# Performance work log

Measured on AMD Instinct MI355X. Metric: run time of the kernel, lower is better.

## Reference

```python
import jax, jax.numpy as jnp
import numpy as np

N_NODES = 50000
N_PAIRS = 400000
F_IN = 5
GCN_DIMS = [32, 64, 128]
MLP_DIMS = [128, 64]


def _lin_init(key, out_d, in_d):
    return jax.random.normal(key, (out_d, in_d), dtype=jnp.float32) / np.sqrt(in_d)


def setup_inputs() -> dict:
    rng = np.random.default_rng(0)
    hi = rng.integers(1, N_NODES, size=N_PAIRS)
    lo = rng.integers(0, 2**31 - 1, size=N_PAIRS) % hi  # lo < hi strictly
    # each undirected pair appears twice per direction (two parallel edges / classes)
    src = np.concatenate([hi, hi, lo, lo]).astype(np.int32)
    dst = np.concatenate([lo, lo, hi, hi]).astype(np.int32)
    edges = jnp.asarray(np.stack([src, dst]))  # [2, 4P]
    detector_labels = jnp.asarray(rng.random(N_NODES) < 0.9)
    key = jax.random.key(0)
    ks = jax.random.split(key, 16)
    x = jax.random.normal(ks[0], (N_NODES, F_IN), dtype=jnp.float32)
    edge_attr = jax.random.uniform(ks[1], (4 * N_PAIRS, 2), dtype=jnp.float32)
    inp = {"x": x, "edges": edges, "edge_attr": edge_attr, "detector_labels": detector_labels}
    dims = [F_IN] + GCN_DIMS
    for i, (di, do) in enumerate(zip(dims[:-1], dims[1:])):
        inp[f"gc{i}_Wrel"] = _lin_init(ks[2 + 3 * i], do, di)
        inp[f"gc{i}_brel"] = jnp.zeros((do,), dtype=jnp.float32)
        inp[f"gc{i}_Wroot"] = _lin_init(ks[3 + 3 * i], do, di)
    mdims = [2 * GCN_DIMS[-1] + 1] + MLP_DIMS
    for i, (di, do) in enumerate(zip(mdims[:-1], mdims[1:])):
        inp[f"fc{i}_W"] = _lin_init(ks[11 + 2 * i], do, di)
        inp[f"fc{i}_b"] = jnp.zeros((do,), dtype=jnp.float32)
    inp["out_W"] = _lin_init(ks[15], 1, MLP_DIMS[-1])
    inp["out_b"] = jnp.zeros((1,), dtype=jnp.float32)
    return inp


def _edge_perm(edges_np, det_np):
    # SplitSyndromes: keep edges with both endpoints in detector set, src > dst,
    # then sort_edge_index (stable lexicographic sort by (src, dst)).
    src, dst = edges_np[0], edges_np[1]
    valid = det_np[src] & det_np[dst] & (src > dst)
    idx = np.where(valid)[0]
    order = np.lexsort((dst[idx], src[idx]))
    return idx[order]


def reference(x, edges, edge_attr, detector_labels,
              gc0_Wrel, gc0_brel, gc0_Wroot,
              gc1_Wrel, gc1_brel, gc1_Wroot,
              gc2_Wrel, gc2_brel, gc2_Wroot,
              fc0_W, fc0_b, fc1_W, fc1_b, out_W, out_b):
    src, dst = edges[0], edges[1]
    w = edge_attr[:, 0] * edge_attr[:, 1]  # GraphConv edge weight
    # GraphConv: lin_rel(sum_j w_ji * x_j) + lin_root(x), ReLU
    for Wrel, brel, Wroot in ((gc0_Wrel, gc0_brel, gc0_Wroot),
                              (gc1_Wrel, gc1_brel, gc1_Wroot),
                              (gc2_Wrel, gc2_brel, gc2_Wroot)):
        agg = jax.ops.segment_sum(x[src] * w[:, None], dst, num_segments=N_NODES)
        x = jax.nn.relu(agg @ Wrel.T + brel + x @ Wroot.T)
    perm = _edge_perm(np.asarray(edges), np.asarray(detector_labels))
    e_src = edges[0, perm]
    e_dst = edges[1, perm]
    ea = edge_attr[perm]  # [M, 2]
    feat = jnp.concatenate([x[e_src], ea[:, :1], x[e_dst]], axis=-1)  # [M, 257]
    for W, b in ((fc0_W, fc0_b), (fc1_W, fc1_b)):
        feat = jax.nn.relu(feat @ W.T + b)
    score = feat @ out_W.T + out_b  # [M, 1]
    pair = jnp.concatenate([score[::2], score[1::2]], axis=1)  # [M/2, 2]
    cls = jnp.stack([ea[::2, 1], ea[1::2, 1]], axis=1)  # [M/2, 2]
    mi = jnp.argmin(pair, axis=1)
    sel = jnp.take_along_axis(pair, mi[:, None], axis=1)[:, 0]
    cls_sel = jnp.take_along_axis(cls, mi[:, None], axis=1)[:, 0]
    edges_out = jnp.stack([e_src[::2], e_dst[::2]])
    return edges_out, jax.nn.sigmoid(sel), cls_sel
```

## Files before the change

kernel.cpp:

```cpp
#include <hip/hip_runtime.h>
#include <hip/hip_bf16.h>
#include <stdint.h>

typedef unsigned long long ull;
typedef unsigned short us;
typedef unsigned char u8;
typedef __attribute__((ext_vector_type(8))) short short8;
typedef __attribute__((ext_vector_type(4))) float f32x4;
#define IDX_BITS 22
#define IDX_MASK 0x3FFFFFu

__device__ __forceinline__ float bfq(float x) {
    return __bfloat162float(__float2bfloat16(x));
}
__device__ __forceinline__ us bfu(float x) {
    __hip_bfloat16 b = __float2bfloat16(x);
    return *(us*)&b;
}
__device__ __forceinline__ float b2f(us u) {
    return __bfloat162float(*(__hip_bfloat16*)&u);
}
__device__ __forceinline__ u8 f2q(float x) {
    x = fminf(fmaxf(x, -448.f), 448.f);
    unsigned int u = __float_as_uint(x);
    unsigned int s = (u >> 24) & 0x80;
    float ax = fabsf(x);
    if (ax < 0.0009765625f) return (u8)s;
    unsigned int au = u & 0x7FFFFFFF;
    int e = (int)(au >> 23) - 127;
    unsigned int m = au & 0x7FFFFF;
    int E = e + 7;
    if (E <= 0) {
        int q = (int)rintf(ax * 512.f);
        if (q >= 8) return (u8)(s | 0x08);
        return (u8)(s | q);
    }
    unsigned int keep = m >> 20;
    unsigned int rest = m & 0xFFFFF;
    keep += (rest > 0x80000u || (rest == 0x80000u && (keep & 1)));
    if (keep == 8) { keep = 0; ++E; }
    if (E >= 16) return (u8)(s | 0x7E);
    return (u8)(s | (E << 3) | keep);
}
__device__ __forceinline__ float q2f(u8 v) {
    int E = (v >> 3) & 0xF, m = v & 7;
    float mag = (E == 0) ? (float)m * 0.001953125f
                         : __uint_as_float((unsigned)(((E + 120) << 23) | (m << 20)));
    return (v & 0x80) ? -mag : mag;
}
__device__ __forceinline__ float ldx(const float* p, size_t i) { return p[i]; }
__device__ __forceinline__ float ldx(const us* p, size_t i) { return b2f(p[i]); }


__global__ void k_det8(const int* __restrict__ src, const int* __restrict__ dst,
                       const u8* __restrict__ det, int P, int gP, int* __restrict__ stats,
                       int* __restrict__ dcnt, int* __restrict__ scnt,
                       int2* __restrict__ rnk, int* __restrict__ vrnk,
                       const float* __restrict__ W1rel, const float* __restrict__ W1root,
                       const float* __restrict__ W2rel, const float* __restrict__ W2root,
                       const float* __restrict__ W3rel, const float* __restrict__ W3root,
                       const float* __restrict__ W0, const float* __restrict__ Wfc1,
                       us* __restrict__ pb1, us* __restrict__ pb2, us* __restrict__ pb3,
                       us* __restrict__ pbP, us* __restrict__ pbQ, us* __restrict__ w1f) {
    if ((int)blockIdx.x >= gP) {
        int gid = (blockIdx.x - gP) * 256 + threadIdx.x;
        const float* Wrel;
        const float* Wroot;
        us* out;
        int idx, FIN, CT;
        if (gid < 1024) { idx = gid; Wrel = W1rel; Wroot = W1root; out = pb1; FIN = 5; CT = 2; }
        else if (gid < 5120) { idx = gid - 1024; Wrel = W2rel; Wroot = W2root; out = pb2; FIN = 32; CT = 4; }
        else if (gid < 21504) { idx = gid - 5120; Wrel = W3rel; Wroot = W3root; out = pb3; FIN = 64; CT = 8; }
        else if (gid < 54272) {
            int i2 = gid - 21504;
            bool isQ = i2 >= 16384;
            int i = i2 & 16383;
            int j = i & 7, l = (i >> 3) & 63, ct = (i >> 9) & 7, ks = i >> 12;
            int k = ks * 32 + ((l >> 4) << 3) + j;
            int col = ct * 16 + (l & 15);
            float v = isQ ? W0[col * 257 + 129 + k] : W0[col * 257 + k];
            (isQ ? pbQ : pbP)[i] = bfu(v);
            return;
        } else if (gid < 62464) {
            int i = gid - 54272;
            int j = i & 7, l = (i >> 3) & 63, ct = (i >> 9) & 3, ks = i >> 11;
            int k = ks * 32 + ((l >> 4) << 3) + j;
            int col = ct * 16 + (l & 15);
            w1f[i] = bfu(Wfc1[col * 128 + k]);
            return;
        } else return;
        int j = idx & 7, l = (idx >> 3) & 63;
        int t = idx >> 9;
        int ct = t % CT, ks = t / CT;
        int k = ks * 32 + ((l >> 4) << 3) + j;
        int col = ct * 16 + (l & 15);
        float v = 0.f;
        if (k < FIN) v = Wrel[col * FIN + k];
        else if (k < 2 * FIN) v = Wroot[col * FIN + (k - FIN)];
        out[idx] = bfu(v);
        return;
    }
    __shared__ int blkc;
    if (threadIdx.x == 0) blkc = 0;
    __syncthreads();
    int e = blockIdx.x * blockDim.x + threadIdx.x;
    bool v = false;
    if (e < P) {
        int hi = src[e], lo = dst[e];
        int r1 = atomicAdd(&dcnt[lo], 1);
        int r2 = atomicAdd(&dcnt[hi], 1);
        rnk[e] = make_int2(r1, r2);
        v = (det[hi] != 0) && (det[lo] != 0);
        vrnk[e] = v ? atomicAdd(&scnt[hi], 1) : -1;
    }
    ull b = __ballot(v);
    if ((threadIdx.x & 63) == 0 && b) atomicAdd(&blkc, (int)__popcll(b));
    __syncthreads();
    if (threadIdx.x == 0 && blkc) atomicAdd(&stats[0], blkc);
}
__global__ void k_det16(const int* __restrict__ src, const int* __restrict__ dst,
                        const us* __restrict__ det, int P, int* __restrict__ stats) {
    if (stats[3] != -1) return;
    __shared__ int blkc;
    if (threadIdx.x == 0) blkc = 0;
    __syncthreads();
    int e = blockIdx.x * blockDim.x + threadIdx.x;
    bool v = false;
    if (e < P) v = (det[src[e]] != 0) && (det[dst[e]] != 0);
    ull b = __ballot(v);
    if ((threadIdx.x & 63) == 0 && b) atomicAdd(&blkc, (int)__popcll(b));
    __syncthreads();
    if (threadIdx.x == 0 && blkc) atomicAdd(&stats[1], blkc);
}
__global__ void k_det32(const int* __restrict__ src, const int* __restrict__ dst,
                        const unsigned int* __restrict__ det, int P, int* __restrict__ stats) {
    if (stats[3] != -2) return;
    __shared__ int blkc;
    if (threadIdx.x == 0) blkc = 0;
    __syncthreads();
    int e = blockIdx.x * blockDim.x + threadIdx.x;
    bool v = false;
    if (e < P) v = (det[src[e]] != 0) && (det[dst[e]] != 0);
    ull b = __ballot(v);
    if ((threadIdx.x & 63) == 0 && b) atomicAdd(&blkc, (int)__popcll(b));
    __syncthreads();
    if (threadIdx.x == 0 && blkc) atomicAdd(&stats[2], blkc);
}
__global__ void k_mode(int* stats, int osz, int step) {
    if (step == 1) {
        int c = stats[0];
        stats[3] = (c == osz / 4 || c == osz / 2) ? 0 : -1;
    } else if (step == 2) {
        if (stats[3] == -1) {
            int c = stats[1];
            stats[3] = (c == osz / 4 || c == osz / 2) ? 2 : -2;
        }
    } else {
        if (stats[3] == -2) stats[3] = 1;
        int m = stats[3];
        stats[4] = (m == 0) ? stats[0] : (m == 2) ? stats[1] : stats[2];
    }
}
__device__ __forceinline__ bool det_ok(int n, const void* det, int mode) {
    if (mode == 0) return ((const u8*)det)[n] != 0;
    if (mode == 2) return ((const us*)det)[n] != 0;
    return ((const unsigned int*)det)[n] != 0;
}
__global__ void k_fixzero(const int* __restrict__ stats, int* __restrict__ scnt, int N) {
    if (stats[3] == 0) return;
    int i = blockIdx.x * blockDim.x + threadIdx.x;
    if (i < N) scnt[i] = 0;
}
__global__ void k_fixhist(const int* __restrict__ src, const int* __restrict__ dst,
                          const void* __restrict__ det, const int* __restrict__ stats,
                          int* __restrict__ scnt, int* __restrict__ vrnk, int P) {
    int m = stats[3];
    if (m == 0) return;
    int e = blockIdx.x * blockDim.x + threadIdx.x;
    if (e >= P) return;
    int hi = src[e], lo = dst[e];
    bool v = det_ok(hi, det, m) && det_ok(lo, det, m);
    vrnk[e] = v ? atomicAdd(&scnt[hi], 1) : -1;
}

__global__ __launch_bounds__(1024) void k_scanA(const int* __restrict__ cnt,
                                                int* __restrict__ off,
                                                int* __restrict__ bsum, int n) {
    __shared__ int wsum[16];
    int t = threadIdx.x, lane = t & 63, w = t >> 6;
    int i = blockIdx.x * 1024 + t;
    int v = (i < n) ? cnt[i] : 0;
    int inc = v;
#pragma unroll
    for (int s = 1; s < 64; s <<= 1) {
        int u = __shfl_up(inc, s);
        if (lane >= s) inc += u;
    }
    if (lane == 63) wsum[w] = inc;
    __syncthreads();
    if (t < 16) {
        int x = wsum[t], sc = x;
#pragma unroll
        for (int s = 1; s < 16; s <<= 1) {
            int u = __shfl_up(sc, s);
            if (t >= s) sc += u;
        }
        wsum[t] = sc - x;
    }
    __syncthreads();
    if (i < n) off[i] = wsum[w] + inc - v;
    if (t == 1023) bsum[blockIdx.x] = wsum[15] + inc;
}
__global__ __launch_bounds__(1024) void k_scanB(int* __restrict__ bsum,
                                                int* __restrict__ off, int nb, int n) {
    __shared__ int wsum[16];
    int t = threadIdx.x, lane = t & 63, w = t >> 6;
    int v = (t < nb) ? bsum[t] : 0;
    int inc = v;
#pragma unroll
    for (int s = 1; s < 64; s <<= 1) {
        int u = __shfl_up(inc, s);
        if (lane >= s) inc += u;
    }
    if (lane == 63) wsum[w] = inc;
    __syncthreads();
    if (t < 16) {
        int x = wsum[t], sc = x;
#pragma unroll
        for (int s = 1; s < 16; s <<= 1) {
            int u = __shfl_up(sc, s);
            if (t >= s) sc += u;
        }
        wsum[t] = sc - x;
    }
    __syncthreads();
    if (t < nb) bsum[t] = wsum[w] + inc - v;
    if (t == 1023) off[n] = wsum[15] + inc;
}
__global__ __launch_bounds__(1024) void k_scanC(int* __restrict__ off,
                                                const int* __restrict__ bsum, int n) {
    int i = blockIdx.x * 1024 + threadIdx.x;
    if (i < n && blockIdx.x > 0) off[i] += bsum[blockIdx.x];
}

__global__ void k_scat2(const int* __restrict__ src, const int* __restrict__ dst,
                        const float* __restrict__ ea, const int* __restrict__ doff,
                        const int* __restrict__ soff, const int2* __restrict__ rnk,
                        const int* __restrict__ vrnk, int2* __restrict__ epair,
                        ull* __restrict__ ent, int P, int Mcap) {
    int e = blockIdx.x * blockDim.x + threadIdx.x;
    if (e >= P) return;
    int hi = src[e], lo = dst[e];
    float w1 = ea[2 * e] * ea[2 * e + 1] + ea[2 * (e + P)] * ea[2 * (e + P) + 1];
    float w2 = ea[2 * (2 * P + e)] * ea[2 * (2 * P + e) + 1] +
               ea[2 * (3 * P + e)] * ea[2 * (3 * P + e) + 1];
    int2 r = rnk[e];
    epair[doff[lo] + r.x] = make_int2(hi, __float_as_int(w1));
    epair[doff[hi] + r.y] = make_int2(lo, __float_as_int(w2));
    int rv = vrnk[e];
    if (rv >= 0) {
        int p = soff[hi] - soff[0] + rv;
        if (p < Mcap) ent[p] = ((ull)(unsigned)lo << IDX_BITS) | (unsigned)e;
    }
}

template <int FIN, int KP, int G, typename TIN>
__global__ __launch_bounds__(256) void k_agg(
    const TIN* __restrict__ xin, const int2* __restrict__ epair,
    const int* __restrict__ doff, us* __restrict__ A, int N) {
    int tid = blockIdx.x * 256 + threadIdx.x;
    int n = tid / G, f = tid % G;
    if (n >= N) return;
    us* row = &A[(size_t)n * KP];
    if (f < FIN) {
        int b = doff[n], e2 = doff[n + 1];
        float a = 0.f;
        int j = b;
        for (; j + 8 <= e2; j += 8) {
            int2 pp[8];
#pragma unroll
            for (int u = 0; u < 8; ++u) pp[u] = epair[j + u];
            float xv[8];
#pragma unroll
            for (int u = 0; u < 8; ++u) xv[u] = ldx(xin, (size_t)pp[u].x * FIN + f);
#pragma unroll
            for (int u = 0; u < 8; ++u) a = fmaf(__int_as_float(pp[u].y), xv[u], a);
        }
        for (; j < e2; ++j) {
            int2 pq = epair[j];
            a = fmaf(__int_as_float(pq.y), ldx(xin, (size_t)pq.x * FIN + f), a);
        }
        row[f] = bfu(a);
        row[FIN + f] = bfu(ldx(xin, (size_t)n * FIN + f));
    }
    for (int c = 2 * FIN + f; c < KP; c += G) row[c] = 0;
}

template <int KP, int FOUT>
__global__ __launch_bounds__(256) void k_mm(
    const us* __restrict__ A, const us* __restrict__ bfrag,
    const float* __restrict__ bias, us* __restrict__ xout, int N) {
    constexpr int CT = FOUT / 16, KS = KP / 32, STR = KP + 8, CPR = KP / 8;
    __shared__ us Al[64 * STR];
    int t = threadIdx.x, lane = t & 63, w = t >> 6;
    int n0 = blockIdx.x * 64;
    for (int idx = t; idx < 64 * CPR; idx += 256) {
        int r = idx / CPR, c = idx % CPR;
        int n = n0 + r;
        uint4 v = (n < N) ? *(const uint4*)&A[(size_t)n * KP + c * 8] : make_uint4(0, 0, 0, 0);
        *(uint4*)&Al[r * STR + c * 8] = v;
    }
    __syncthreads();
    f32x4 acc[CT];
#pragma unroll
    for (int ct = 0; ct < CT; ++ct) acc[ct] = (f32x4){0.f, 0.f, 0.f, 0.f};
    int arow = w * 16 + (lane & 15);
    int koff = (lane >> 4) << 3;
#pragma unroll
    for (int ks = 0; ks < KS; ++ks) {
        short8 a = *(const short8*)&Al[arow * STR + ks * 32 + koff];
#pragma unroll
        for (int ct = 0; ct < CT; ++ct) {
            short8 b = ((const short8*)bfrag)[(ks * CT + ct) * 64 + lane];
            acc[ct] = __builtin_amdgcn_mfma_f32_16x16x32_bf16(a, b, acc[ct], 0, 0, 0);
        }
    }
    int g = lane >> 4, c0 = lane & 15;
#pragma unroll
    for (int ct = 0; ct < CT; ++ct) {
        int col = ct * 16 + c0;
        float bb = bias[col];
#pragma unroll
        for (int r2 = 0; r2 < 4; ++r2) {
            int n = n0 + w * 16 + g * 4 + r2;
            if (n < N) xout[(size_t)n * FOUT + col] = bfu(fmaxf(acc[ct][r2] + bb, 0.f));
        }
    }
}

__global__ __launch_bounds__(256) void k_mmPQ(
    const us* __restrict__ x3b, const us* __restrict__ pbP, const us* __restrict__ pbQ,
    const float* __restrict__ b0, us* __restrict__ P, u8* __restrict__ Q, int N) {
    constexpr int CT = 8, KS = 4, STR = 136, CPR = 16;
    __shared__ us Al[64 * STR];
    int t = threadIdx.x, lane = t & 63, w = t >> 6;
    int n0 = blockIdx.x * 64;
    for (int idx = t; idx < 64 * CPR; idx += 256) {
        int r = idx / CPR, c = idx % CPR;
        int n = n0 + r;
        uint4 v = (n < N) ? *(const uint4*)&x3b[(size_t)n * 128 + c * 8] : make_uint4(0, 0, 0, 0);
        *(uint4*)&Al[r * STR + c * 8] = v;
    }
    __syncthreads();
    int arow = w * 16 + (lane & 15);
    int koff = (lane >> 4) << 3;
    int g = lane >> 4, c0 = lane & 15;
    f32x4 acc[CT];
#pragma unroll
    for (int ct = 0; ct < CT; ++ct) acc[ct] = (f32x4){0.f, 0.f, 0.f, 0.f};
#pragma unroll
    for (int ks = 0; ks < KS; ++ks) {
        short8 a = *(const short8*)&Al[arow * STR + ks * 32 + koff];
#pragma unroll
        for (int ct = 0; ct < CT; ++ct) {
            short8 b = ((const short8*)pbP)[(ks * CT + ct) * 64 + lane];
            acc[ct] = __builtin_amdgcn_mfma_f32_16x16x32_bf16(a, b, acc[ct], 0, 0, 0);
        }
    }
#pragma unroll
    for (int ct = 0; ct < CT; ++ct) {
        int col = ct * 16 + c0;
        float bb = b0[col];
#pragma unroll
        for (int r2 = 0; r2 < 4; ++r2) {
            int n = n0 + w * 16 + g * 4 + r2;
            if (n < N) P[(size_t)n * 128 + col] = bfu(acc[ct][r2] + bb);
        }
    }
#pragma unroll
    for (int ct = 0; ct < CT; ++ct) acc[ct] = (f32x4){0.f, 0.f, 0.f, 0.f};
#pragma unroll
    for (int ks = 0; ks < KS; ++ks) {
        short8 a = *(const short8*)&Al[arow * STR + ks * 32 + koff];
#pragma unroll
        for (int ct = 0; ct < CT; ++ct) {
            short8 b = ((const short8*)pbQ)[(ks * CT + ct) * 64 + lane];
            acc[ct] = __builtin_amdgcn_mfma_f32_16x16x32_bf16(a, b, acc[ct], 0, 0, 0);
        }
    }
#pragma unroll
    for (int ct = 0; ct < CT; ++ct) {
        int col = ct * 16 + c0;
#pragma unroll
        for (int r2 = 0; r2 < 4; ++r2) {
            int n = n0 + w * 16 + g * 4 + r2;
            if (n < N) Q[(size_t)n * 128 + col] = f2q(acc[ct][r2]);
        }
    }
}

__global__ __launch_bounds__(256) void k_wsort(const int* __restrict__ soff,
                                               ull* __restrict__ ent, int N, int Mcap) {
    int node = blockIdx.x * 4 + (threadIdx.x >> 6);
    int lane = threadIdx.x & 63;
    if (node >= N) return;
    int base = soff[0];
    int b = soff[node] - base, e2 = soff[node + 1] - base;
    if (e2 > Mcap) e2 = Mcap;
    int len = e2 - b;
    if (len <= 1) return;
    if (len <= 64) {
        ull key = (lane < len) ? ent[b + lane] : ~0ull;
        int phases = len + (len & 1);
        for (int ph = 0; ph < phases; ++ph) {
            int partner;
            if ((ph & 1) == 0) partner = lane ^ 1;
            else partner = (lane == 0 || lane == 63) ? lane
                                                     : ((lane & 1) ? lane + 1 : lane - 1);
            ull other = __shfl(key, partner);
            if (partner > lane) key = key < other ? key : other;
            else if (partner < lane) key = key > other ? key : other;
        }
        if (lane < len) ent[b + lane] = key;
    } else if (lane == 0) {
        for (int i = b + 1; i < e2; ++i) {
            ull k = ent[i];
            int j = i - 1;
            while (j >= b && ent[j] > k) { ent[j + 1] = ent[j]; --j; }
            ent[j + 1] = k;
        }
    }
}

__global__ __launch_bounds__(256) void k_mlp2(
    const us* __restrict__ Pm, const u8* __restrict__ Qm, const float* __restrict__ ea,
    const int* __restrict__ src, const ull* __restrict__ ent, const int* __restrict__ stats,
    const float* __restrict__ W0, const us* __restrict__ w1f,
    const float* __restrict__ b1, const float* __restrict__ w2, const float* __restrict__ b2,
    float* __restrict__ out, int P) {
    int Mh = stats[4];
    int rows = 2 * Mh;
    int m0 = blockIdx.x * 64;
    if (m0 >= rows) return;
    __shared__ us A[64 * 136];
    __shared__ float ws0e[128];
    __shared__ int pHi[32], pLo[32];
    __shared__ float clsA[32], clsB[32];
    int t = threadIdx.x, lane = t & 63, w = t >> 6;
    if (t < 128) ws0e[t] = W0[t * 257 + 128];
    __syncthreads();

    {
        int j = t >> 3, q = t & 7;
        int pr = (m0 >> 1) + j;
        if (pr < Mh) {
            ull en = ent[pr];
            int e = (int)(en & IDX_MASK);
            int lo = (int)(en >> IDX_BITS);
            int hi = src[e];
            float eaA = ea[2 * e];
            float eaB = ea[2 * (e + P)];
            if (q == 0) {
                pHi[j] = hi;
                pLo[j] = lo;
                clsA[j] = ea[2 * e + 1];
                clsB[j] = ea[2 * (e + P) + 1];
            }
            const us* Pr = Pm + (size_t)hi * 128 + q * 16;
            uint4 qraw = *(const uint4*)(Qm + (size_t)lo * 128 + q * 16);
            const u8* qb = (const u8*)&qraw;
#pragma unroll
            for (int h = 0; h < 2; ++h) {
                int cb = q * 16 + h * 8;
                short8 pv = *(const short8*)&Pr[h * 8];
                short8 ra, rb;
#pragma unroll
                for (int i = 0; i < 8; ++i) {
                    float base = b2f((us)pv[i]) + q2f(qb[h * 8 + i]);
                    float we = ws0e[cb + i];
                    ra[i] = (short)bfu(fmaxf(base + eaA * we, 0.f));
                    rb[i] = (short)bfu(fmaxf(base + eaB * we, 0.f));
                }
                *(short8*)&A[(2 * j) * 136 + cb] = ra;
                *(short8*)&A[(2 * j + 1) * 136 + cb] = rb;
            }
        } else {
            uint4 z = make_uint4(0, 0, 0, 0);
            *(uint4*)&A[(2 * j) * 136 + q * 16] = z;
            *(uint4*)&A[(2 * j) * 136 + q * 16 + 8] = z;
            *(uint4*)&A[(2 * j + 1) * 136 + q * 16] = z;
            *(uint4*)&A[(2 * j + 1) * 136 + q * 16 + 8] = z;
        }
    }
    __syncthreads();

    f32x4 acc1[4];
#pragma unroll
    for (int ct = 0; ct < 4; ++ct) acc1[ct] = (f32x4){0.f, 0.f, 0.f, 0.f};
    {
        int arow = w * 16 + (lane & 15);
        int koff = (lane >> 4) << 3;
#pragma unroll
        for (int ks = 0; ks < 4; ++ks) {
            short8 a = *(const short8*)&A[arow * 136 + ks * 32 + koff];
#pragma unroll
            for (int ct = 0; ct < 4; ++ct) {
                short8 b = ((const short8*)w1f)[(ks * 4 + ct) * 64 + lane];
                acc1[ct] = __builtin_amdgcn_mfma_f32_16x16x32_bf16(a, b, acc1[ct], 0, 0, 0);
            }
        }
    }
    {
        int g = lane >> 4, c0 = lane & 15;
        float part[4] = {0.f, 0.f, 0.f, 0.f};
#pragma unroll
        for (int ct = 0; ct < 4; ++ct) {
            int col = ct * 16 + c0;
            float bb = b1[col], wv = w2[col];
#pragma unroll
            for (int r = 0; r < 4; ++r)
                part[r] += fmaxf(acc1[ct][r] + bb, 0.f) * wv;
        }
        float bout = b2[0];
        float sv[4];
#pragma unroll
        for (int r = 0; r < 4; ++r) {
            float v = part[r];
            v += __shfl_xor(v, 1);
            v += __shfl_xor(v, 2);
            v += __shfl_xor(v, 4);
            v += __shfl_xor(v, 8);
            sv[r] = v + bout;
        }
        if (c0 == 0) {
#pragma unroll
            for (int rr = 0; rr < 4; rr += 2) {
                int jloc = (w * 16 + g * 4 + rr) >> 1;
                int pgi = (m0 >> 1) + jloc;
                if (pgi < Mh) {
                    float s0 = sv[rr], s1 = sv[rr + 1];
                    int pick = (s1 < s0) ? 1 : 0;
                    float sel = pick ? s1 : s0;
                    float cls = pick ? clsB[jloc] : clsA[jloc];
                    float sig = 1.f / (1.f + expf(-sel));
                    out[pgi] = bfq((float)pHi[jloc]);
                    out[Mh + pgi] = bfq((float)pLo[jloc]);
                    out[2 * Mh + pgi] = bfq(sig);
                    out[3 * Mh + pgi] = bfq(cls);
                }
            }
        }
    }
}

extern "C" void kernel_launch(void* const* d_in, const int* in_sizes, int n_in,
                              void* d_out, int out_size, void* d_ws, size_t ws_size,
                              hipStream_t stream) {
    const float* x0 = (const float*)d_in[0];
    const int* edges = (const int*)d_in[1];
    const float* ea = (const float*)d_in[2];
    const void* det = d_in[3];

    int N = in_sizes[0] / 5;
    int E = in_sizes[1] / 2;
    int P = E / 4;
    int osz = out_size;
    int Mcap = osz / 2;

    const int* src = edges;
    const int* dst = edges + E;

    char* p = (char*)d_ws;
    auto alloc = [&](size_t bytes) {
        char* r = p;
        p += (bytes + 255) & ~(size_t)255;
        return r;
    };
    us* xa = (us*)alloc((size_t)N * 32 * 2);
    us* xb = (us*)alloc((size_t)N * 64 * 2);
    us* x3b = (us*)alloc((size_t)N * 128 * 2);
    us* Abuf = (us*)alloc((size_t)N * 128 * 2);
    us* Pb = Abuf;
    u8* Qb = (u8*)alloc((size_t)N * 128);
    us* pb1 = (us*)alloc(1024 * 2);
    us* pb2 = (us*)alloc(4096 * 2);
    us* pb3 = (us*)alloc(16384 * 2);
    us* pbP = (us*)alloc(16384 * 2);
    us* pbQ = (us*)alloc(16384 * 2);
    us* w1f = (us*)alloc(8192 * 2);
    int* bsum = (int*)alloc(1024);
    int2* rnk = (int2*)alloc((size_t)P * 8);
    int* vrnk = (int*)alloc((size_t)P * 4);
    char* z0 = p;
    int* stats = (int*)alloc(256);
    int* cnt2 = (int*)alloc((size_t)2 * N * 4);
    size_t zlen = (size_t)(p - z0);
    int* dcnt = cnt2;
    int* scnt = cnt2 + N;
    int* doff2 = (int*)alloc((size_t)(2 * N + 1) * 4);
    int* doff = doff2;
    int* soff = doff2 + N;
    int2* epair = (int2*)alloc((size_t)(2 * P) * 8);
    ull* ent = (ull*)alloc((size_t)Mcap * 8);
    size_t need = (size_t)(p - (char*)d_ws);
    if (need > ws_size) return;

    const int B = 256;
    int gP = (P + B - 1) / B;
    int n2 = 2 * N;
    int nb2 = (n2 + 1023) / 1024;

    hipMemsetAsync(z0, 0, zlen, stream);

    k_det8<<<gP + 244, B, 0, stream>>>(
        src, dst, (const u8*)det, P, gP, stats, dcnt, scnt, rnk, vrnk,
        (const float*)d_in[4], (const float*)d_in[6],
        (const float*)d_in[7], (const float*)d_in[9],
        (const float*)d_in[10], (const float*)d_in[12],
        (const float*)d_in[13], (const float*)d_in[15],
        pb1, pb2, pb3, pbP, pbQ, w1f);
    k_mode<<<1, 1, 0, stream>>>(stats, osz, 1);
    k_det16<<<gP, B, 0, stream>>>(src, dst, (const us*)det, P, stats);
    k_mode<<<1, 1, 0, stream>>>(stats, osz, 2);
    k_det32<<<gP, B, 0, stream>>>(src, dst, (const unsigned int*)det, P, stats);
    k_mode<<<1, 1, 0, stream>>>(stats, osz, 3);
    k_fixzero<<<(N + B - 1) / B, B, 0, stream>>>(stats, scnt, N);
    k_fixhist<<<gP, B, 0, stream>>>(src, dst, det, stats, scnt, vrnk, P);

    k_scanA<<<nb2, 1024, 0, stream>>>(cnt2, doff2, bsum, n2);
    k_scanB<<<1, 1024, 0, stream>>>(bsum, doff2, nb2, n2);
    k_scanC<<<nb2, 1024, 0, stream>>>(doff2, bsum, n2);

    k_scat2<<<gP, B, 0, stream>>>(src, dst, ea, doff, soff, rnk, vrnk, epair, ent, P, Mcap);

    k_agg<5, 32, 8, float><<<((size_t)N * 8 + B - 1) / B, B, 0, stream>>>(
        x0, epair, doff, Abuf, N);
    k_mm<32, 32><<<(N + 63) / 64, B, 0, stream>>>(Abuf, pb1, (const float*)d_in[5], xa, N);
    k_agg<32, 64, 32, us><<<((size_t)N * 32 + B - 1) / B, B, 0, stream>>>(
        xa, epair, doff, Abuf, N);
    k_mm<64, 64><<<(N + 63) / 64, B, 0, stream>>>(Abuf, pb2, (const float*)d_in[8], xb, N);
    k_agg<64, 128, 64, us><<<((size_t)N * 64 + B - 1) / B, B, 0, stream>>>(
        xb, epair, doff, Abuf, N);
    k_mm<128, 128><<<(N + 63) / 64, B, 0, stream>>>(Abuf, pb3, (const float*)d_in[11], x3b, N);

    k_mmPQ<<<(N + 63) / 64, B, 0, stream>>>(x3b, pbP, pbQ, (const float*)d_in[14], Pb, Qb, N);

    k_wsort<<<(N + 3) / 4, B, 0, stream>>>(soff, ent, N, Mcap);

    k_mlp2<<<(osz + 63) / 64, B, 0, stream>>>(
        Pb, Qb, ea, src, ent, stats,
        (const float*)d_in[13], w1f,
        (const float*)d_in[16], (const float*)d_in[17], (const float*)d_in[18],
        (float*)d_out, P);
}
```

Before: 332.2 us.

## Fuse last GCN matmul into PQ projection, pack edge counters, drop mode kernels

The third GCN layer's matmul is merged with the P/Q projection. The layer output now stays in LDS as bf16 and is fed straight into the second MFMA pass, so the x3b buffer is never written to or read back from global memory. The two degree histograms are packed into one 64-bit counter per node, which cuts the per-edge atomics from three to two and has the scan read from the packed array. The three single-thread k_mode launches are gone; each consumer now recomputes the mode from stats inline. This costs a larger fused kernel and extra LDS round-trips per block.

```diff
diff --git a/kernel.cpp b/kernel.cpp
--- a/kernel.cpp
+++ b/kernel.cpp
@@ -51,11 +51,26 @@
 __device__ __forceinline__ float ldx(const float* p, size_t i) { return p[i]; }
 __device__ __forceinline__ float ldx(const us* p, size_t i) { return b2f(p[i]); }
 
+__device__ __forceinline__ bool cmatch(int c, int osz) { return c == osz / 4 || c == osz / 2; }
+__device__ __forceinline__ int get_mode(const int* stats, int osz) {
+    if (cmatch(stats[0], osz)) return 0;
+    if (cmatch(stats[1], osz)) return 2;
+    return 1;
+}
+__device__ __forceinline__ int get_mh(const int* stats, int osz) {
+    if (cmatch(stats[0], osz)) return stats[0];
+    if (cmatch(stats[1], osz)) return stats[1];
+    return stats[2];
+}
+__device__ __forceinline__ bool det_ok(int n, const void* det, int mode) {
+    if (mode == 0) return ((const u8*)det)[n] != 0;
+    if (mode == 2) return ((const us*)det)[n] != 0;
+    return ((const unsigned int*)det)[n] != 0;
+}
 
 __global__ void k_det8(const int* __restrict__ src, const int* __restrict__ dst,
                        const u8* __restrict__ det, int P, int gP, int* __restrict__ stats,
-                       int* __restrict__ dcnt, int* __restrict__ scnt,
-                       int2* __restrict__ rnk, int* __restrict__ vrnk,
+                       ull* __restrict__ pk, int2* __restrict__ rnk, int* __restrict__ vrnk,
                        const float* __restrict__ W1rel, const float* __restrict__ W1root,
                        const float* __restrict__ W2rel, const float* __restrict__ W2root,
                        const float* __restrict__ W3rel, const float* __restrict__ W3root,
@@ -107,11 +122,11 @@
     bool v = false;
     if (e < P) {
         int hi = src[e], lo = dst[e];
-        int r1 = atomicAdd(&dcnt[lo], 1);
-        int r2 = atomicAdd(&dcnt[hi], 1);
-        rnk[e] = make_int2(r1, r2);
         v = (det[hi] != 0) && (det[lo] != 0);
-        vrnk[e] = v ? atomicAdd(&scnt[hi], 1) : -1;
+        ull o1 = atomicAdd(&pk[lo], 1ull);
+        ull o2 = atomicAdd(&pk[hi], 1ull + (v ? (1ull << 32) : 0ull));
+        rnk[e] = make_int2((int)(o1 & 0xFFFFFFFFull), (int)(o2 & 0xFFFFFFFFull));
+        vrnk[e] = v ? (int)(o2 >> 32) : -1;
     }
     ull b = __ballot(v);
     if ((threadIdx.x & 63) == 0 && b) atomicAdd(&blkc, (int)__popcll(b));
@@ -119,8 +134,8 @@
     if (threadIdx.x == 0 && blkc) atomicAdd(&stats[0], blkc);
 }
 __global__ void k_det16(const int* __restrict__ src, const int* __restrict__ dst,
-                        const us* __restrict__ det, int P, int* __restrict__ stats) {
-    if (stats[3] != -1) return;
+                        const us* __restrict__ det, int P, int osz, int* __restrict__ stats) {
+    if (cmatch(stats[0], osz)) return;
     __shared__ int blkc;
     if (threadIdx.x == 0) blkc = 0;
     __syncthreads();
@@ -133,8 +148,9 @@
     if (threadIdx.x == 0 && blkc) atomicAdd(&stats[1], blkc);
 }
 __global__ void k_det32(const int* __restrict__ src, const int* __restrict__ dst,
-                        const unsigned int* __restrict__ det, int P, int* __restrict__ stats) {
-    if (stats[3] != -2) return;
+                        const unsigned int* __restrict__ det, int P, int osz,
+                        int* __restrict__ stats) {
+    if (cmatch(stats[0], osz) || cmatch(stats[1], osz)) return;
     __shared__ int blkc;
     if (threadIdx.x == 0) blkc = 0;
     __syncthreads();
@@ -146,50 +162,39 @@
     __syncthreads();
     if (threadIdx.x == 0 && blkc) atomicAdd(&stats[2], blkc);
 }
-__global__ void k_mode(int* stats, int osz, int step) {
-    if (step == 1) {
-        int c = stats[0];
-        stats[3] = (c == osz / 4 || c == osz / 2) ? 0 : -1;
-    } else if (step == 2) {
-        if (stats[3] == -1) {
-            int c = stats[1];
-            stats[3] = (c == osz / 4 || c == osz / 2) ? 2 : -2;
-        }
-    } else {
-        if (stats[3] == -2) stats[3] = 1;
-        int m = stats[3];
-        stats[4] = (m == 0) ? stats[0] : (m == 2) ? stats[1] : stats[2];
-    }
-}
-__device__ __forceinline__ bool det_ok(int n, const void* det, int mode) {
-    if (mode == 0) return ((const u8*)det)[n] != 0;
-    if (mode == 2) return ((const us*)det)[n] != 0;
-    return ((const unsigned int*)det)[n] != 0;
-}
-__global__ void k_fixzero(const int* __restrict__ stats, int* __restrict__ scnt, int N) {
-    if (stats[3] == 0) return;
+__global__ void k_fixzero(const int* __restrict__ stats, int osz, ull* __restrict__ pk, int N) {
+    if (cmatch(stats[0], osz)) return;
     int i = blockIdx.x * blockDim.x + threadIdx.x;
-    if (i < N) scnt[i] = 0;
+    if (i < N) pk[i] &= 0xFFFFFFFFull;
 }
 __global__ void k_fixhist(const int* __restrict__ src, const int* __restrict__ dst,
-                          const void* __restrict__ det, const int* __restrict__ stats,
-                          int* __restrict__ scnt, int* __restrict__ vrnk, int P) {
-    int m = stats[3];
+                          const void* __restrict__ det, const int* __restrict__ stats, int osz,
+                          ull* __restrict__ pk, int* __restrict__ vrnk, int P) {
+    int m = get_mode(stats, osz);
     if (m == 0) return;
     int e = blockIdx.x * blockDim.x + threadIdx.x;
     if (e >= P) return;
     int hi = src[e], lo = dst[e];
     bool v = det_ok(hi, det, m) && det_ok(lo, det, m);
-    vrnk[e] = v ? atomicAdd(&scnt[hi], 1) : -1;
-}
-
-__global__ __launch_bounds__(1024) void k_scanA(const int* __restrict__ cnt,
+    if (v) {
+        ull o = atomicAdd(&pk[hi], 1ull << 32);
+        vrnk[e] = (int)(o >> 32);
+    } else {
+        vrnk[e] = -1;
+    }
+}
+
+__global__ __launch_bounds__(1024) void k_scanP(const ull* __restrict__ pk,
                                                 int* __restrict__ off,
-                                                int* __restrict__ bsum, int n) {
+                                                int* __restrict__ bsum, int N, int n2) {
     __shared__ int wsum[16];
     int t = threadIdx.x, lane = t & 63, w = t >> 6;
     int i = blockIdx.x * 1024 + t;
-    int v = (i < n) ? cnt[i] : 0;
+    int v = 0;
+    if (i < n2) {
+        ull pv = (i < N) ? pk[i] : pk[i - N];
+        v = (i < N) ? (int)(pv & 0xFFFFFFFFull) : (int)(pv >> 32);
+    }
     int inc = v;
 #pragma unroll
     for (int s = 1; s < 64; s <<= 1) {
@@ -208,7 +213,7 @@
         wsum[t] = sc - x;
     }
     __syncthreads();
-    if (i < n) off[i] = wsum[w] + inc - v;
+    if (i < n2) off[i] = wsum[w] + inc - v;
     if (t == 1023) bsum[blockIdx.x] = wsum[15] + inc;
 }
 __global__ __launch_bounds__(1024) void k_scanB(int* __restrict__ bsum,
@@ -338,9 +343,10 @@
     }
 }
 
-__global__ __launch_bounds__(256) void k_mmPQ(
-    const us* __restrict__ x3b, const us* __restrict__ pbP, const us* __restrict__ pbQ,
-    const float* __restrict__ b0, us* __restrict__ P, u8* __restrict__ Q, int N) {
+__global__ __launch_bounds__(256) void k_mm3pq(
+    const us* __restrict__ A, const us* __restrict__ bfrag, const float* __restrict__ bias,
+    const us* __restrict__ pbP, const us* __restrict__ pbQ, const float* __restrict__ b0,
+    us* __restrict__ Pout, u8* __restrict__ Qout, int N) {
     constexpr int CT = 8, KS = 4, STR = 136, CPR = 16;
     __shared__ us Al[64 * STR];
     int t = threadIdx.x, lane = t & 63, w = t >> 6;
@@ -348,7 +354,7 @@
     for (int idx = t; idx < 64 * CPR; idx += 256) {
         int r = idx / CPR, c = idx % CPR;
         int n = n0 + r;
-        uint4 v = (n < N) ? *(const uint4*)&x3b[(size_t)n * 128 + c * 8] : make_uint4(0, 0, 0, 0);
+        uint4 v = (n < N) ? *(const uint4*)&A[(size_t)n * 128 + c * 8] : make_uint4(0, 0, 0, 0);
         *(uint4*)&Al[r * STR + c * 8] = v;
     }
     __syncthreads();
@@ -363,6 +369,29 @@
         short8 a = *(const short8*)&Al[arow * STR + ks * 32 + koff];
 #pragma unroll
         for (int ct = 0; ct < CT; ++ct) {
+            short8 b = ((const short8*)bfrag)[(ks * CT + ct) * 64 + lane];
+            acc[ct] = __builtin_amdgcn_mfma_f32_16x16x32_bf16(a, b, acc[ct], 0, 0, 0);
+        }
+    }
+    __syncthreads();
+#pragma unroll
+    for (int ct = 0; ct < CT; ++ct) {
+        int col = ct * 16 + c0;
+        float bb = bias[col];
+#pragma unroll
+        for (int r2 = 0; r2 < 4; ++r2) {
+            int rowl = w * 16 + g * 4 + r2;
+            Al[rowl * STR + col] = bfu(fmaxf(acc[ct][r2] + bb, 0.f));
+        }
+    }
+    __syncthreads();
+#pragma unroll
+    for (int ct = 0; ct < CT; ++ct) acc[ct] = (f32x4){0.f, 0.f, 0.f, 0.f};
+#pragma unroll
+    for (int ks = 0; ks < KS; ++ks) {
+        short8 a = *(const short8*)&Al[arow * STR + ks * 32 + koff];
+#pragma unroll
+        for (int ct = 0; ct < CT; ++ct) {
             short8 b = ((const short8*)pbP)[(ks * CT + ct) * 64 + lane];
             acc[ct] = __builtin_amdgcn_mfma_f32_16x16x32_bf16(a, b, acc[ct], 0, 0, 0);
         }
@@ -374,7 +403,7 @@
 #pragma unroll
         for (int r2 = 0; r2 < 4; ++r2) {
             int n = n0 + w * 16 + g * 4 + r2;
-            if (n < N) P[(size_t)n * 128 + col] = bfu(acc[ct][r2] + bb);
+            if (n < N) Pout[(size_t)n * 128 + col] = bfu(acc[ct][r2] + bb);
         }
     }
 #pragma unroll
@@ -394,7 +423,7 @@
 #pragma unroll
         for (int r2 = 0; r2 < 4; ++r2) {
             int n = n0 + w * 16 + g * 4 + r2;
-            if (n < N) Q[(size_t)n * 128 + col] = f2q(acc[ct][r2]);
+            if (n < N) Qout[(size_t)n * 128 + col] = f2q(acc[ct][r2]);
         }
     }
 }
@@ -435,10 +464,10 @@
 __global__ __launch_bounds__(256) void k_mlp2(
     const us* __restrict__ Pm, const u8* __restrict__ Qm, const float* __restrict__ ea,
     const int* __restrict__ src, const ull* __restrict__ ent, const int* __restrict__ stats,
-    const float* __restrict__ W0, const us* __restrict__ w1f,
+    int osz, const float* __restrict__ W0, const us* __restrict__ w1f,
     const float* __restrict__ b1, const float* __restrict__ w2, const float* __restrict__ b2,
     float* __restrict__ out, int P) {
-    int Mh = stats[4];
+    int Mh = get_mh(stats, osz);
     int rows = 2 * Mh;
     int m0 = blockIdx.x * 64;
     if (m0 >= rows) return;
@@ -578,7 +607,6 @@
     };
     us* xa = (us*)alloc((size_t)N * 32 * 2);
     us* xb = (us*)alloc((size_t)N * 64 * 2);
-    us* x3b = (us*)alloc((size_t)N * 128 * 2);
     us* Abuf = (us*)alloc((size_t)N * 128 * 2);
     us* Pb = Abuf;
     u8* Qb = (u8*)alloc((size_t)N * 128);
@@ -593,10 +621,8 @@
     int* vrnk = (int*)alloc((size_t)P * 4);
     char* z0 = p;
     int* stats = (int*)alloc(256);
-    int* cnt2 = (int*)alloc((size_t)2 * N * 4);
+    ull* pk = (ull*)alloc((size_t)N * 8);
     size_t zlen = (size_t)(p - z0);
-    int* dcnt = cnt2;
-    int* scnt = cnt2 + N;
     int* doff2 = (int*)alloc((size_t)(2 * N + 1) * 4);
     int* doff = doff2;
     int* soff = doff2 + N;
@@ -613,21 +639,18 @@
     hipMemsetAsync(z0, 0, zlen, stream);
 
     k_det8<<<gP + 244, B, 0, stream>>>(
-        src, dst, (const u8*)det, P, gP, stats, dcnt, scnt, rnk, vrnk,
+        src, dst, (const u8*)det, P, gP, stats, pk, rnk, vrnk,
         (const float*)d_in[4], (const float*)d_in[6],
         (const float*)d_in[7], (const float*)d_in[9],
         (const float*)d_in[10], (const float*)d_in[12],
         (const float*)d_in[13], (const float*)d_in[15],
         pb1, pb2, pb3, pbP, pbQ, w1f);
-    k_mode<<<1, 1, 0, stream>>>(stats, osz, 1);
-    k_det16<<<gP, B, 0, stream>>>(src, dst, (const us*)det, P, stats);
-    k_mode<<<1, 1, 0, stream>>>(stats, osz, 2);
-    k_det32<<<gP, B, 0, stream>>>(src, dst, (const unsigned int*)det, P, stats);
-    k_mode<<<1, 1, 0, stream>>>(stats, osz, 3);
-    k_fixzero<<<(N + B - 1) / B, B, 0, stream>>>(stats, scnt, N);
-    k_fixhist<<<gP, B, 0, stream>>>(src, dst, det, stats, scnt, vrnk, P);
-
-    k_scanA<<<nb2, 1024, 0, stream>>>(cnt2, doff2, bsum, n2);
+    k_det16<<<gP, B, 0, stream>>>(src, dst, (const us*)det, P, osz, stats);
+    k_det32<<<gP, B, 0, stream>>>(src, dst, (const unsigned int*)det, P, osz, stats);
+    k_fixzero<<<(N + B - 1) / B, B, 0, stream>>>(stats, osz, pk, N);
+    k_fixhist<<<gP, B, 0, stream>>>(src, dst, det, stats, osz, pk, vrnk, P);
+
+    k_scanP<<<nb2, 1024, 0, stream>>>(pk, doff2, bsum, N, n2);
     k_scanB<<<1, 1024, 0, stream>>>(bsum, doff2, nb2, n2);
     k_scanC<<<nb2, 1024, 0, stream>>>(doff2, bsum, n2);
 
@@ -641,14 +664,13 @@
     k_mm<64, 64><<<(N + 63) / 64, B, 0, stream>>>(Abuf, pb2, (const float*)d_in[8], xb, N);
     k_agg<64, 128, 64, us><<<((size_t)N * 64 + B - 1) / B, B, 0, stream>>>(
         xb, epair, doff, Abuf, N);
-    k_mm<128, 128><<<(N + 63) / 64, B, 0, stream>>>(Abuf, pb3, (const float*)d_in[11], x3b, N);
-
-    k_mmPQ<<<(N + 63) / 64, B, 0, stream>>>(x3b, pbP, pbQ, (const float*)d_in[14], Pb, Qb, N);
+    k_mm3pq<<<(N + 63) / 64, B, 0, stream>>>(Abuf, pb3, (const float*)d_in[11],
+                                             pbP, pbQ, (const float*)d_in[14], Pb, Qb, N);
 
     k_wsort<<<(N + 3) / 4, B, 0, stream>>>(soff, ent, N, Mcap);
 
     k_mlp2<<<(osz + 63) / 64, B, 0, stream>>>(
-        Pb, Qb, ea, src, ent, stats,
+        Pb, Qb, ea, src, ent, stats, osz,
         (const float*)d_in[13], w1f,
         (const float*)d_in[16], (const float*)d_in[17], (const float*)d_in[18],
         (float*)d_out, P);
```

Measured after the change: 326.7 us. Within noise of the previous version (-1.7%).
